# Performance work log

Measured on AMD Instinct MI355X. Metric: run time of the kernel, lower is better.

Reference implementation:

```python
import jax, jax.numpy as jnp
import numpy as np

B, F, H, W = 1, 6, 20, 26
S = F * H * W            # 3120 tokens
DIM, NH, HD = 1536, 12, 128
C = HD // 2              # 64 rotary channels
T_C = C - 2 * (C // 3)   # 22 temporal channels
H_C = C // 3             # 21
W_C = C // 3             # 21
LOCAL_FRAMES = 4         # local_attn_size (in frames)
SINK_FRAMES = 1          # sink_size (in frames)
EPS = 1e-6
MAX_POS = 1024


def _angle_table(n_ch):
    inv = 1.0 / (10000.0 ** (np.arange(n_ch, dtype=np.float64) / n_ch))
    return np.outer(np.arange(MAX_POS, dtype=np.float64), inv)


def setup_inputs() -> dict:
    key = jax.random.key(0)
    ks = jax.random.split(key, 8)
    sc = 0.02
    ang = np.concatenate([_angle_table(T_C), _angle_table(H_C), _angle_table(W_C)], axis=1)  # [1024, 64]
    return {
        "x": jax.random.normal(ks[0], (B, S, DIM), jnp.float32),
        "seq_lens": jnp.array([S], jnp.int32),
        "grid_sizes": jnp.array([[F, H, W]], jnp.int32),
        "freqs_cos": jnp.asarray(np.cos(ang), jnp.float32),
        "freqs_sin": jnp.asarray(np.sin(ang), jnp.float32),
        "Wq": jax.random.normal(ks[1], (DIM, DIM), jnp.float32) * sc,
        "bq": jnp.zeros((DIM,), jnp.float32),
        "Wk": jax.random.normal(ks[2], (DIM, DIM), jnp.float32) * sc,
        "bk": jnp.zeros((DIM,), jnp.float32),
        "Wv": jax.random.normal(ks[3], (DIM, DIM), jnp.float32) * sc,
        "bv": jnp.zeros((DIM,), jnp.float32),
        "Wo": jax.random.normal(ks[4], (DIM, DIM), jnp.float32) * sc,
        "bo": jnp.zeros((DIM,), jnp.float32),
        "gq": jnp.ones((DIM,), jnp.float32),
        "gk": jnp.ones((DIM,), jnp.float32),
    }


def _rms_norm(x, g):
    # WanRMSNorm: x * rsqrt(mean(x^2) + eps) * weight
    return x * jax.lax.rsqrt(jnp.mean(x * x, axis=-1, keepdims=True) + EPS) * g


def _rope_apply(x, freqs_cos, freqs_sin):
    # x: [B, S, NH, HD]; per-token 3D (f,h,w) rotary on consecutive pairs.
    pos = jnp.arange(S)
    f = pos // (H * W)
    hh = (pos // W) % H
    ww = pos % W
    cos_t, cos_h, cos_w = freqs_cos[:, :T_C], freqs_cos[:, T_C:T_C + H_C], freqs_cos[:, T_C + H_C:]
    sin_t, sin_h, sin_w = freqs_sin[:, :T_C], freqs_sin[:, T_C:T_C + H_C], freqs_sin[:, T_C + H_C:]
    cos = jnp.concatenate([cos_t[f], cos_h[hh], cos_w[ww]], axis=-1)[None, :, None, :]  # [1,S,1,C]
    sin = jnp.concatenate([sin_t[f], sin_h[hh], sin_w[ww]], axis=-1)[None, :, None, :]
    xp = x.reshape(B, S, NH, C, 2)
    xr, xi = xp[..., 0], xp[..., 1]
    out = jnp.stack([xr * cos - xi * sin, xr * sin + xi * cos], axis=-1)
    return out.reshape(B, S, NH, HD)


def _block_mask():
    # frame-causal + local window (in frames) + sink frames: [S, S] bool
    fid = jnp.arange(S) // (H * W)
    fi, fj = fid[:, None], fid[None, :]
    return (fj <= fi) & ((fi - fj < LOCAL_FRAMES) | (fj < SINK_FRAMES))


def reference(x, seq_lens, grid_sizes, freqs_cos, freqs_sin,
              Wq, bq, Wk, bk, Wv, bv, Wo, bo, gq, gk):
    q = _rms_norm(x @ Wq + bq, gq).reshape(B, S, NH, HD)
    k = _rms_norm(x @ Wk + bk, gk).reshape(B, S, NH, HD)
    v = (x @ Wv + bv).reshape(B, S, NH, HD)
    rq = _rope_apply(q, freqs_cos, freqs_sin)
    rk = _rope_apply(k, freqs_cos, freqs_sin)
    scale = 1.0 / jnp.sqrt(jnp.asarray(HD, x.dtype))
    scores = jnp.einsum('bind,bjnd->bnij', rq, rk) * scale  # [B,NH,S,S]
    scores = jnp.where(_block_mask()[None, None], scores, jnp.finfo(scores.dtype).min)
    attn = jax.nn.softmax(scores, axis=-1)
    out = jnp.einsum('bnij,bjnd->bind', attn, v).reshape(B, S, DIM)
    return out @ Wo + bo
```

## Files before the change

### kernel.cpp

```cpp
#include <hip/hip_runtime.h>
#include <hip/hip_bf16.h>
#include <stdint.h>

typedef short v8s __attribute__((ext_vector_type(8)));
typedef float v4f __attribute__((ext_vector_type(4)));
typedef unsigned short u16;

#define S_LEN 3120
#define DIMN 1536
#define NHEAD 12
#define HDIM 128
#define FRM 520
#define NT128 25
#define TASKS_PH 86
#define TOTAL_TASKS 1032
#define SCALE_QK 0.088388347648318447f
#define MAXOFF 12.0f

__device__ __forceinline__ v4f mfma16(v8s a, v8s b, v4f c) {
  return __builtin_amdgcn_mfma_f32_16x16x32_bf16(a, b, c, 0, 0, 0);
}
__device__ __forceinline__ float b2f(u16 u) {
  union { float f; unsigned int i; } x; x.i = ((unsigned int)u) << 16; return x.f;
}
__device__ __forceinline__ u16 f2b(float f) {
  union { float f; unsigned int i; } x; x.f = f;
  unsigned int r = x.i + 0x7FFFu + ((x.i >> 16) & 1u);
  return (u16)(r >> 16);
}
__device__ __forceinline__ void async16(const void* g, void* l) {
  __builtin_amdgcn_global_load_lds(
      (__attribute__((address_space(1))) const void*)g,
      (__attribute__((address_space(3))) void*)l, 16, 0, 0);
}

__global__ void detect_dtype(const u16* __restrict__ w, int* __restrict__ flag) {
  __shared__ int sh;
  int t = threadIdx.x;
  if (t == 0) sh = 0;
  __syncthreads();
  u16 m0 = (u16)(w[2 * t] & 0x7FFF);
  u16 m1 = (u16)(w[2 * t + 1] & 0x7FFF);
  if (m0 >= 0x4480 || m1 >= 0x4480) atomicOr(&sh, 1);
  __syncthreads();
  if (t == 0) *flag = sh;
}

struct ConvArgs { const void* src[9]; u16* dst[9]; int n[9]; };
__global__ __launch_bounds__(256) void convert_all(ConvArgs a, const int* __restrict__ flag) {
  int id = blockIdx.y;
  int n = a.n[id];
  int isf = *flag;
  const float* sf = (const float*)a.src[id];
  const u16* sb = (const u16*)a.src[id];
  u16* d = a.dst[id];
  for (int i = blockIdx.x * 256 + threadIdx.x; i < n; i += gridDim.x * 256)
    d[i] = isf ? f2b(sf[i]) : sb[i];
}

struct TPArgs { const void* in[4]; u16* out[4]; };
__global__ __launch_bounds__(256) void transpose_conv4(TPArgs a, const int* __restrict__ flag) {
  __shared__ u16 tile[32][33];
  int z = blockIdx.z;
  const float* inf = (const float*)a.in[z];
  const u16* inb = (const u16*)a.in[z];
  u16* out = a.out[z];
  int isf = *flag;
  int t = threadIdx.x, tx = t & 31, ty = t >> 5;
  int gr0 = blockIdx.y * 32, gc0 = blockIdx.x * 32;
#pragma unroll
  for (int i = 0; i < 4; ++i) {
    int r = ty + i * 8;
    size_t idx = (size_t)(gr0 + r) * DIMN + gc0 + tx;
    tile[r][tx] = isf ? f2b(inf[idx]) : inb[idx];
  }
  __syncthreads();
#pragma unroll
  for (int i = 0; i < 4; ++i) {
    int r = ty + i * 8;
    out[(size_t)(gc0 + r) * DIMN + gr0 + tx] = tile[tx][r];
  }
}

__global__ __launch_bounds__(256) void transpose16(const u16* __restrict__ in,
                                                   u16* __restrict__ out,
                                                   int rows, int cols) {
  __shared__ u16 tile[32][33];
  int t = threadIdx.x;
  int tx = t & 31, ty = t >> 5;
  int gr0 = blockIdx.y * 32, gc0 = blockIdx.x * 32;
#pragma unroll
  for (int i = 0; i < 4; ++i) {
    int r = ty + i * 8;
    int gr = gr0 + r, gc = gc0 + tx;
    if (gr < rows && gc < cols) tile[r][tx] = in[(size_t)gr * cols + gc];
  }
  __syncthreads();
#pragma unroll
  for (int i = 0; i < 4; ++i) {
    int r = ty + i * 8;
    int orow = gc0 + r, ocol = gr0 + tx;
    if (orow < cols && ocol < rows) out[(size_t)orow * rows + ocol] = tile[tx][r];
  }
}

template <int MT>
__global__ __launch_bounds__(256) void gemm3(
    const u16* __restrict__ A,
    const u16* BT0, const u16* BT1, const u16* BT2,
    const u16* b0, const u16* b1, const u16* b2,
    void* C0, void* C1, void* C2, int M, const int* __restrict__ flag, int dyn) {
  const u16* BT; const u16* bias; void* C;
  if (blockIdx.z == 0)      { BT = BT0; bias = b0; C = C0; }
  else if (blockIdx.z == 1) { BT = BT1; bias = b1; C = C1; }
  else                      { BT = BT2; bias = b2; C = C2; }
  int f32out = dyn ? *flag : 0;
  __shared__ __align__(16) short As[MT * 64];
  __shared__ __align__(16) short Bs[128 * 64];
  int t = threadIdx.x, w = t >> 6, l = t & 63;
  int ln = l & 15, lg = l >> 4;
  int m0 = blockIdx.y * MT, n0 = blockIdx.x * 128;
  int lr = l >> 3;
  int gl = (l & 7) ^ lr;
  constexpr int ACH = MT / 32;
  const u16* gAp[ACH]; short* lAp[ACH];
#pragma unroll
  for (int i = 0; i < ACH; ++i) {
    int c = w * ACH + i;
    int arow = min(m0 + c * 8 + lr, M - 1);
    gAp[i] = A + (size_t)arow * DIMN + gl * 8;
    lAp[i] = As + c * 512;
  }
  const u16* gBp[4]; short* lBp[4];
#pragma unroll
  for (int i = 0; i < 4; ++i) {
    int c = w * 4 + i;
    int brow = n0 + c * 8 + lr;
    gBp[i] = BT + (size_t)brow * DIMN + gl * 8;
    lBp[i] = Bs + c * 512;
  }
  constexpr int NJ = (MT == 128) ? 4 : 2;
  int wm = (MT == 128) ? (w & 1) : 0;
  int wn = (MT == 128) ? (w >> 1) : w;
  int aoff[2][4], boff[2][NJ];
#pragma unroll
  for (int ks = 0; ks < 2; ++ks) {
#pragma unroll
    for (int i = 0; i < 4; ++i) {
      int ar = wm * 64 + i * 16 + ln;
      aoff[ks][i] = ar * 64 + (((ks * 4 + lg) ^ (ar & 7)) * 8);
    }
#pragma unroll
    for (int j = 0; j < NJ; ++j) {
      int br = wn * (NJ * 16) + j * 16 + ln;
      boff[ks][j] = br * 64 + (((ks * 4 + lg) ^ (br & 7)) * 8);
    }
  }
  v4f acc[4][NJ] = {};
  for (int k0 = 0; k0 < DIMN; k0 += 64) {
    __syncthreads();
#pragma unroll
    for (int i = 0; i < ACH; ++i) async16(gAp[i] + k0, lAp[i]);
#pragma unroll
    for (int i = 0; i < 4; ++i) async16(gBp[i] + k0, lBp[i]);
    __syncthreads();
#pragma unroll
    for (int ks = 0; ks < 2; ++ks) {
      v8s af[4], bfr[NJ];
#pragma unroll
      for (int i = 0; i < 4; ++i) af[i] = *(const v8s*)(As + aoff[ks][i]);
#pragma unroll
      for (int j = 0; j < NJ; ++j) bfr[j] = *(const v8s*)(Bs + boff[ks][j]);
#pragma unroll
      for (int i = 0; i < 4; ++i)
#pragma unroll
        for (int j = 0; j < NJ; ++j) acc[i][j] = mfma16(af[i], bfr[j], acc[i][j]);
    }
  }
#pragma unroll
  for (int i = 0; i < 4; ++i) {
    int rb = m0 + wm * 64 + i * 16 + lg * 4;
#pragma unroll
    for (int j = 0; j < NJ; ++j) {
      int col = n0 + wn * (NJ * 16) + j * 16 + ln;
      float bv = b2f(bias[col]);
#pragma unroll
      for (int r = 0; r < 4; ++r) {
        int grow = rb + r;
        if (grow < M) {
          size_t idx = (size_t)grow * DIMN + col;
          float val = acc[i][j][r] + bv;
          if (f32out) ((float*)C)[idx] = val;
          else        ((u16*)C)[idx] = f2b(val);
        }
      }
    }
  }
}

__global__ __launch_bounds__(256) void norm_rope(u16* __restrict__ Q, u16* __restrict__ K,
                                                 const u16* __restrict__ gq,
                                                 const u16* __restrict__ gk,
                                                 const u16* __restrict__ fcos,
                                                 const u16* __restrict__ fsin) {
  int s = blockIdx.x;
  u16* base = (blockIdx.y == 0 ? Q : K) + (size_t)s * DIMN;
  const u16* g = (blockIdx.y == 0) ? gq : gk;
  int t = threadIdx.x;
  int e = t * 6;
  float x[6];
#pragma unroll
  for (int i = 0; i < 6; ++i) x[i] = b2f(base[e + i]);
  float ss = 0.f;
#pragma unroll
  for (int i = 0; i < 6; ++i) ss += x[i] * x[i];
#pragma unroll
  for (int off = 32; off > 0; off >>= 1) ss += __shfl_xor(ss, off);
  __shared__ float red[4];
  if ((t & 63) == 0) red[t >> 6] = ss;
  __syncthreads();
  float tot = red[0] + red[1] + red[2] + red[3];
  float rs = rsqrtf(tot * (1.0f / DIMN) + 1e-6f);
  int f = s / FRM;
  int hh = (s / 26) % 20;
  int ww = s % 26;
#pragma unroll
  for (int u = 0; u < 3; ++u) {
    int e0 = e + 2 * u;
    int c = (e0 & 127) >> 1;
    int p = (c < 22) ? f : ((c < 43) ? hh : ww);
    float co = b2f(fcos[p * 64 + c]);
    float si = b2f(fsin[p * 64 + c]);
    float xr = x[2 * u] * rs * b2f(g[e0]);
    float xi = x[2 * u + 1] * rs * b2f(g[e0 + 1]);
    base[e0]     = f2b(xr * co - xi * si);
    base[e0 + 1] = f2b(xr * si + xi * co);
  }
}

__global__ __launch_bounds__(256) void attn_block(const u16* __restrict__ Q,
                                                  const u16* __restrict__ K,
                                                  const u16* __restrict__ VT,
                                                  u16* __restrict__ Po,
                                                  float* __restrict__ Pl) {
  __shared__ __align__(16) short Ks[64 * 128];
  __shared__ __align__(16) short Vs[128 * 64];
  __shared__ __align__(16) short Pt[4][32 * 72];
  int t = threadIdx.x, w = t >> 6, l = t & 63;
  int ln = l & 15, lg = l >> 4;
  int task = blockIdx.x;
  int head = task / TASKS_PH, tid = task % TASKS_PH;
  int tile = 0, frame = 0;
  {
    int acc = 0;
    for (tile = 0; tile < NT128; ++tile) {
      int q0t = tile * 128;
      int f_lo = q0t / FRM;
      int f_hi = min(q0t + 127, S_LEN - 1) / FRM;
      int fstart = max(0, f_lo - 3);
      int sink = fstart > 0;
      int nf = f_hi - fstart + 1 + sink;
      if (tid < acc + nf) {
        int c = tid - acc;
        frame = sink ? (c == 0 ? 0 : fstart + c - 1) : (fstart + c);
        break;
      }
      acc += nf;
    }
  }
  int q0 = tile * 128 + w * 32;
  v8s qf[2][4];
  bool rowok[2][4];
#pragma unroll
  for (int g = 0; g < 2; ++g) {
    int row = min(q0 + g * 16 + ln, S_LEN - 1);
    const u16* qp = Q + (size_t)row * DIMN + head * HDIM + lg * 8;
#pragma unroll
    for (int c = 0; c < 4; ++c) qf[g][c] = *(const v8s*)(qp + c * 32);
#pragma unroll
    for (int r = 0; r < 4; ++r) {
      int qr = q0 + g * 16 + lg * 4 + r;
      int fi = (qr < S_LEN) ? qr / FRM : -1;
      rowok[g][r] = (frame <= fi) && ((fi - frame) < 4 || frame == 0);
    }
  }
  float lsum[2][4] = {};
  v4f o[2][8] = {};
  int kbeg = frame * FRM, kend = kbeg + FRM;
  for (int kb = kbeg; kb < kend; kb += 64) {
    __syncthreads();
#pragma unroll
    for (int i = 0; i < 4; ++i) {
      int c = w * 4 + i;
      int n = c * 64 + l;
      int r = n >> 4;
      int gl = (n & 15) ^ (r & 15);
      int krow = min(kb + r, S_LEN - 1);
      async16((const char*)K + (size_t)krow * (DIMN * 2) + head * 256 + gl * 16,
              (char*)Ks + c * 1024);
    }
#pragma unroll
    for (int i = 0; i < 4; ++i) {
      int c = w * 4 + i;
      int n = c * 64 + l;
      int d = n >> 3;
      int gl = (n & 7) ^ (d & 7);
      async16((const char*)VT + (size_t)(head * HDIM + d) * (S_LEN * 2) + (size_t)kb * 2 + gl * 16,
              (char*)Vs + c * 1024);
    }
    __syncthreads();
    v4f s[2][4] = {};
#pragma unroll
    for (int kg = 0; kg < 4; ++kg) {
      int kr = kg * 16 + ln;
#pragma unroll
      for (int c = 0; c < 4; ++c) {
        v8s kf = *(const v8s*)(Ks + kr * 128 + (((c * 4 + lg) ^ ln) * 8));
        s[0][kg] = mfma16(qf[0][c], kf, s[0][kg]);
        s[1][kg] = mfma16(qf[1][c], kf, s[1][kg]);
      }
    }
#pragma unroll
    for (int g = 0; g < 2; ++g)
#pragma unroll
      for (int kg = 0; kg < 4; ++kg) {
        bool jv = (kb + kg * 16 + ln) < kend;
#pragma unroll
        for (int r = 0; r < 4; ++r) {
          float p = (rowok[g][r] && jv) ? __expf(s[g][kg][r] * SCALE_QK - MAXOFF) : 0.f;
          lsum[g][r] += p;
          Pt[w][(g * 16 + lg * 4 + r) * 72 + kg * 16 + ln] = f2b(p);
        }
      }
#pragma unroll
    for (int kc = 0; kc < 2; ++kc) {
      v8s pf0 = *(const v8s*)(&Pt[w][ln * 72 + kc * 32 + lg * 8]);
      v8s pf1 = *(const v8s*)(&Pt[w][(16 + ln) * 72 + kc * 32 + lg * 8]);
#pragma unroll
      for (int d = 0; d < 8; ++d) {
        int rr = d * 16 + ln;
        v8s vf = *(const v8s*)(Vs + rr * 64 + (((kc * 4 + lg) ^ (ln & 7)) * 8));
        o[0][d] = mfma16(pf0, vf, o[0][d]);
        o[1][d] = mfma16(pf1, vf, o[1][d]);
      }
    }
  }
#pragma unroll
  for (int g = 0; g < 2; ++g)
#pragma unroll
    for (int r = 0; r < 4; ++r) {
      float v = lsum[g][r];
      v += __shfl_xor(v, 1);
      v += __shfl_xor(v, 2);
      v += __shfl_xor(v, 4);
      v += __shfl_xor(v, 8);
      lsum[g][r] = v;
    }
  size_t pbase = (size_t)task * (128 * 128);
#pragma unroll
  for (int g = 0; g < 2; ++g)
#pragma unroll
    for (int d = 0; d < 8; ++d)
#pragma unroll
      for (int r = 0; r < 4; ++r) {
        int lrow = w * 32 + g * 16 + lg * 4 + r;
        Po[pbase + lrow * 128 + d * 16 + ln] = f2b(o[g][d][r]);
      }
  if (ln == 0) {
#pragma unroll
    for (int g = 0; g < 2; ++g)
#pragma unroll
      for (int r = 0; r < 4; ++r)
        Pl[task * 128 + w * 32 + g * 16 + lg * 4 + r] = lsum[g][r];
  }
}

__global__ __launch_bounds__(256) void attn_combine(const u16* __restrict__ Po,
                                                    const float* __restrict__ Pl,
                                                    u16* __restrict__ Oa) {
  int tile = blockIdx.x, h = blockIdx.y;
  int accv = 0, nf = 0;
  for (int q = 0; q < NT128; ++q) {
    int q0t = q * 128;
    int f_lo = q0t / FRM;
    int f_hi = min(q0t + 127, S_LEN - 1) / FRM;
    int fstart = max(0, f_lo - 3);
    int sink = fstart > 0;
    nf = f_hi - fstart + 1 + sink;
    if (q == tile) break;
    accv += nf;
  }
  int base = h * TASKS_PH + accv;
  int t = threadIdx.x;
  int row = t >> 1, seg = (t & 1) * 64;
  int grow = tile * 128 + row;
  if (grow >= S_LEN) return;
  float lsum = 0.f;
  float ao[64];
#pragma unroll
  for (int j = 0; j < 64; ++j) ao[j] = 0.f;
  for (int c = 0; c < nf; ++c) {
    int task = base + c;
    lsum += Pl[task * 128 + row];
    const u16* p = Po + (size_t)task * 16384 + row * 128 + seg;
#pragma unroll
    for (int v = 0; v < 8; ++v) {
      v8s x = *(const v8s*)(p + v * 8);
#pragma unroll
      for (int j = 0; j < 8; ++j) ao[v * 8 + j] += b2f((u16)x[j]);
    }
  }
  float inv = 1.0f / lsum;
  u16* dst = Oa + (size_t)grow * DIMN + h * HDIM + seg;
#pragma unroll
  for (int v = 0; v < 8; ++v) {
    v8s res;
#pragma unroll
    for (int j = 0; j < 8; ++j) res[j] = (short)f2b(ao[v * 8 + j] * inv);
    *(v8s*)(dst + v * 8) = res;
  }
}

extern "C" void kernel_launch(void* const* d_in, const int* in_sizes, int n_in,
                              void* d_out, int out_size, void* d_ws, size_t ws_size,
                              hipStream_t stream) {
  (void)n_in; (void)out_size; (void)ws_size;
  int* flag = (int*)d_ws;
  u16* ws = (u16*)d_ws;
  size_t off = 16;
  const size_t SD = (size_t)S_LEN * DIMN;
  const size_t WW = (size_t)DIMN * DIMN;
  const size_t NPO = (size_t)TOTAL_TASKS * 128 * 128;
  auto alloc = [&](size_t n) { u16* p = ws + off; off += (n + 7) & ~(size_t)7; return p; };
  u16* Xc  = alloc(SD);
  u16* Fc  = alloc(65536);
  u16* Fs  = alloc(65536);
  u16* bqc = alloc(1536); u16* bkc = alloc(1536); u16* bvc = alloc(1536); u16* boc = alloc(1536);
  u16* gqc = alloc(1536); u16* gkc = alloc(1536);
  u16* Qr = alloc(SD); u16* Kr = alloc(SD); u16* Vr = alloc(SD); u16* Oa = alloc(SD);
  u16* WoT = alloc(WW);
  u16* WqT = alloc(WW); u16* WkT = alloc(WW); u16* WvT = alloc(WW);
  alloc(NPO - 3 * WW);
  float* Pl = (float*)alloc((size_t)TOTAL_TASKS * 128 * 2);
  u16* Po = WqT;
  u16* VT = Xc;

  detect_dtype<<<1, 256, 0, stream>>>((const u16*)d_in[5], flag);

  ConvArgs ca;
  const int srcIdx[9] = {0, 3, 4, 6, 8, 10, 12, 13, 14};
  u16* dsts[9] = {Xc, Fc, Fs, bqc, bkc, bvc, boc, gqc, gkc};
  for (int i = 0; i < 9; ++i) {
    ca.src[i] = d_in[srcIdx[i]];
    ca.dst[i] = dsts[i];
    ca.n[i] = in_sizes[srcIdx[i]];
  }
  convert_all<<<dim3(512, 9), 256, 0, stream>>>(ca, flag);

  TPArgs tp;
  tp.in[0] = d_in[5];  tp.out[0] = WqT;
  tp.in[1] = d_in[7];  tp.out[1] = WkT;
  tp.in[2] = d_in[9];  tp.out[2] = WvT;
  tp.in[3] = d_in[11]; tp.out[3] = WoT;
  dim3 b256(256);
  transpose_conv4<<<dim3(48, 48, 4), b256, 0, stream>>>(tp, flag);
  gemm3<64><<<dim3(12, 49, 3), b256, 0, stream>>>(Xc, WqT, WkT, WvT, bqc, bkc, bvc,
                                                  Qr, Kr, Vr, S_LEN, flag, 0);
  norm_rope<<<dim3(S_LEN, 2), b256, 0, stream>>>(Qr, Kr, gqc, gkc, Fc, Fs);
  transpose16<<<dim3(48, 98), b256, 0, stream>>>(Vr, VT, S_LEN, DIMN);
  attn_block<<<dim3(TOTAL_TASKS), b256, 0, stream>>>(Qr, Kr, VT, Po, Pl);
  attn_combine<<<dim3(NT128, NHEAD), b256, 0, stream>>>(Po, Pl, Oa);
  gemm3<64><<<dim3(12, 49, 1), b256, 0, stream>>>(Oa, WoT, WoT, WoT, boc, boc, boc,
                                                  d_out, d_out, d_out, S_LEN, flag, 1);
}
```

Measured before the change: 401.7 us.

## Shrink attention query tiles to 64 rows and key steps to 32; merge prep kernels

Attention tasks now cover 64-query tiles with 2 waves (128 threads) instead of 128-query tiles with 4 waves, and iterate keys in 32-row steps with smaller LDS buffers. This roughly doubles the task count to improve load balance and occupancy, and shrinks the partial-output buffers. The sum is accumulated from the truncated bf16 probabilities so it matches the values fed to the MFMA. The conversion and transpose prep kernels are merged into one launch. Per-task Q loads and K/V reuse drop, so more global traffic per output is the risk.

New measurement: 375.2 us. -6.6%, faster.

```diff
diff --git a/kernel.cpp b/kernel.cpp
--- a/kernel.cpp
+++ b/kernel.cpp
@@ -11,9 +11,10 @@
 #define NHEAD 12
 #define HDIM 128
 #define FRM 520
-#define NT128 25
-#define TASKS_PH 86
-#define TOTAL_TASKS 1032
+#define NT64 49
+#define T64_PH 166
+#define TOT64 1992
+#define NSTEP32 17
 #define SCALE_QK 0.088388347648318447f
 #define MAXOFF 12.0f
 
@@ -46,39 +47,43 @@
   if (t == 0) *flag = sh;
 }
 
-struct ConvArgs { const void* src[9]; u16* dst[9]; int n[9]; };
-__global__ __launch_bounds__(256) void convert_all(ConvArgs a, const int* __restrict__ flag) {
-  int id = blockIdx.y;
-  int n = a.n[id];
+struct PrepArgs {
+  const void* tin[4]; u16* tout[4];
+  const void* csrc[9]; u16* cdst[9]; int cn[9];
+};
+__global__ __launch_bounds__(256) void prep(PrepArgs a, const int* __restrict__ flag) {
   int isf = *flag;
-  const float* sf = (const float*)a.src[id];
-  const u16* sb = (const u16*)a.src[id];
-  u16* d = a.dst[id];
-  for (int i = blockIdx.x * 256 + threadIdx.x; i < n; i += gridDim.x * 256)
-    d[i] = isf ? f2b(sf[i]) : sb[i];
-}
-
-struct TPArgs { const void* in[4]; u16* out[4]; };
-__global__ __launch_bounds__(256) void transpose_conv4(TPArgs a, const int* __restrict__ flag) {
-  __shared__ u16 tile[32][33];
   int z = blockIdx.z;
-  const float* inf = (const float*)a.in[z];
-  const u16* inb = (const u16*)a.in[z];
-  u16* out = a.out[z];
-  int isf = *flag;
-  int t = threadIdx.x, tx = t & 31, ty = t >> 5;
-  int gr0 = blockIdx.y * 32, gc0 = blockIdx.x * 32;
-#pragma unroll
-  for (int i = 0; i < 4; ++i) {
-    int r = ty + i * 8;
-    size_t idx = (size_t)(gr0 + r) * DIMN + gc0 + tx;
-    tile[r][tx] = isf ? f2b(inf[idx]) : inb[idx];
-  }
-  __syncthreads();
-#pragma unroll
-  for (int i = 0; i < 4; ++i) {
-    int r = ty + i * 8;
-    out[(size_t)(gc0 + r) * DIMN + gr0 + tx] = tile[tx][r];
+  int t = threadIdx.x;
+  if (z < 4) {
+    __shared__ u16 tile[32][33];
+    const float* inf = (const float*)a.tin[z];
+    const u16* inb = (const u16*)a.tin[z];
+    u16* out = a.tout[z];
+    int tx = t & 31, ty = t >> 5;
+    int gr0 = blockIdx.y * 32, gc0 = blockIdx.x * 32;
+#pragma unroll
+    for (int i = 0; i < 4; ++i) {
+      int r = ty + i * 8;
+      size_t idx = (size_t)(gr0 + r) * DIMN + gc0 + tx;
+      tile[r][tx] = isf ? f2b(inf[idx]) : inb[idx];
+    }
+    __syncthreads();
+#pragma unroll
+    for (int i = 0; i < 4; ++i) {
+      int r = ty + i * 8;
+      out[(size_t)(gc0 + r) * DIMN + gr0 + tx] = tile[tx][r];
+    }
+  } else {
+    int id = z - 4;
+    int n = a.cn[id];
+    const float* sf = (const float*)a.csrc[id];
+    const u16* sb = (const u16*)a.csrc[id];
+    u16* d = a.cdst[id];
+    int bidx = blockIdx.y * gridDim.x + blockIdx.x;
+    int stride = gridDim.x * gridDim.y * 256;
+    for (int i = bidx * 256 + t; i < n; i += stride)
+      d[i] = isf ? f2b(sf[i]) : sb[i];
   }
 }
 
@@ -238,25 +243,25 @@
   }
 }
 
-__global__ __launch_bounds__(256) void attn_block(const u16* __restrict__ Q,
+__global__ __launch_bounds__(128) void attn_block(const u16* __restrict__ Q,
                                                   const u16* __restrict__ K,
                                                   const u16* __restrict__ VT,
                                                   u16* __restrict__ Po,
                                                   float* __restrict__ Pl) {
-  __shared__ __align__(16) short Ks[64 * 128];
-  __shared__ __align__(16) short Vs[128 * 64];
-  __shared__ __align__(16) short Pt[4][32 * 72];
+  __shared__ __align__(16) short Ks[32 * 128];
+  __shared__ __align__(16) short Vs[128 * 32];
+  __shared__ __align__(16) short Pt[2][32 * 40];
   int t = threadIdx.x, w = t >> 6, l = t & 63;
   int ln = l & 15, lg = l >> 4;
   int task = blockIdx.x;
-  int head = task / TASKS_PH, tid = task % TASKS_PH;
+  int head = task / T64_PH, tid = task % T64_PH;
   int tile = 0, frame = 0;
   {
     int acc = 0;
-    for (tile = 0; tile < NT128; ++tile) {
-      int q0t = tile * 128;
+    for (tile = 0; tile < NT64; ++tile) {
+      int q0t = tile * 64;
       int f_lo = q0t / FRM;
-      int f_hi = min(q0t + 127, S_LEN - 1) / FRM;
+      int f_hi = min(q0t + 63, S_LEN - 1) / FRM;
       int fstart = max(0, f_lo - 3);
       int sink = fstart > 0;
       int nf = f_hi - fstart + 1 + sink;
@@ -268,7 +273,7 @@
       acc += nf;
     }
   }
-  int q0 = tile * 128 + w * 32;
+  int q0 = tile * 64 + w * 32;
   v8s qf[2][4];
   bool rowok[2][4];
 #pragma unroll
@@ -287,35 +292,34 @@
   float lsum[2][4] = {};
   v4f o[2][8] = {};
   int kbeg = frame * FRM, kend = kbeg + FRM;
-  for (int kb = kbeg; kb < kend; kb += 64) {
+  int kr_i[4], kgl_i[4], vd_i[4], vgl_i[4];
+#pragma unroll
+  for (int i = 0; i < 4; ++i) {
+    int n = (w * 4 + i) * 64 + l;
+    kr_i[i] = n >> 4;
+    kgl_i[i] = (n & 15) ^ (kr_i[i] & 15);
+    vd_i[i] = n >> 2;
+    vgl_i[i] = (n & 3) ^ (vd_i[i] & 3);
+  }
+  const u16* Kb = K + head * HDIM;
+  for (int it = 0; it < NSTEP32; ++it) {
+    int kb = kbeg + it * 32;
     __syncthreads();
 #pragma unroll
     for (int i = 0; i < 4; ++i) {
-      int c = w * 4 + i;
-      int n = c * 64 + l;
-      int r = n >> 4;
-      int gl = (n & 15) ^ (r & 15);
-      int krow = min(kb + r, S_LEN - 1);
-      async16((const char*)K + (size_t)krow * (DIMN * 2) + head * 256 + gl * 16,
-              (char*)Ks + c * 1024);
-    }
-#pragma unroll
-    for (int i = 0; i < 4; ++i) {
-      int c = w * 4 + i;
-      int n = c * 64 + l;
-      int d = n >> 3;
-      int gl = (n & 7) ^ (d & 7);
-      async16((const char*)VT + (size_t)(head * HDIM + d) * (S_LEN * 2) + (size_t)kb * 2 + gl * 16,
-              (char*)Vs + c * 1024);
+      int krow = min(kb + kr_i[i], S_LEN - 1);
+      async16(Kb + (size_t)krow * DIMN + kgl_i[i] * 8,
+              (char*)Ks + (size_t)(w * 4 + i) * 1024);
+      async16(VT + (size_t)(head * HDIM + vd_i[i]) * S_LEN + kb + vgl_i[i] * 8,
+              (char*)Vs + (size_t)(w * 4 + i) * 1024);
     }
     __syncthreads();
-    v4f s[2][4] = {};
-#pragma unroll
-    for (int kg = 0; kg < 4; ++kg) {
-      int kr = kg * 16 + ln;
+    v4f s[2][2] = {};
+#pragma unroll
+    for (int kg = 0; kg < 2; ++kg) {
 #pragma unroll
       for (int c = 0; c < 4; ++c) {
-        v8s kf = *(const v8s*)(Ks + kr * 128 + (((c * 4 + lg) ^ ln) * 8));
+        v8s kf = *(const v8s*)(&Ks[(kg * 16 + ln) * 128 + (((c * 4 + lg) ^ ln) * 8)]);
         s[0][kg] = mfma16(qf[0][c], kf, s[0][kg]);
         s[1][kg] = mfma16(qf[1][c], kf, s[1][kg]);
       }
@@ -323,26 +327,24 @@
 #pragma unroll
     for (int g = 0; g < 2; ++g)
 #pragma unroll
-      for (int kg = 0; kg < 4; ++kg) {
+      for (int kg = 0; kg < 2; ++kg) {
         bool jv = (kb + kg * 16 + ln) < kend;
 #pragma unroll
         for (int r = 0; r < 4; ++r) {
           float p = (rowok[g][r] && jv) ? __expf(s[g][kg][r] * SCALE_QK - MAXOFF) : 0.f;
-          lsum[g][r] += p;
-          Pt[w][(g * 16 + lg * 4 + r) * 72 + kg * 16 + ln] = f2b(p);
+          unsigned int bi = __float_as_uint(p) & 0xffff0000u;
+          lsum[g][r] += __uint_as_float(bi);
+          Pt[w][(g * 16 + lg * 4 + r) * 40 + kg * 16 + ln] = (u16)(bi >> 16);
         }
       }
-#pragma unroll
-    for (int kc = 0; kc < 2; ++kc) {
-      v8s pf0 = *(const v8s*)(&Pt[w][ln * 72 + kc * 32 + lg * 8]);
-      v8s pf1 = *(const v8s*)(&Pt[w][(16 + ln) * 72 + kc * 32 + lg * 8]);
-#pragma unroll
-      for (int d = 0; d < 8; ++d) {
-        int rr = d * 16 + ln;
-        v8s vf = *(const v8s*)(Vs + rr * 64 + (((kc * 4 + lg) ^ (ln & 7)) * 8));
-        o[0][d] = mfma16(pf0, vf, o[0][d]);
-        o[1][d] = mfma16(pf1, vf, o[1][d]);
-      }
+    v8s pf0 = *(const v8s*)(&Pt[w][ln * 40 + lg * 8]);
+    v8s pf1 = *(const v8s*)(&Pt[w][(16 + ln) * 40 + lg * 8]);
+#pragma unroll
+    for (int d = 0; d < 8; ++d) {
+      int rr = d * 16 + ln;
+      v8s vf = *(const v8s*)(&Vs[rr * 32 + ((lg ^ (rr & 3)) * 8)]);
+      o[0][d] = mfma16(pf0, vf, o[0][d]);
+      o[1][d] = mfma16(pf1, vf, o[1][d]);
     }
   }
 #pragma unroll
@@ -356,7 +358,7 @@
       v += __shfl_xor(v, 8);
       lsum[g][r] = v;
     }
-  size_t pbase = (size_t)task * (128 * 128);
+  size_t pbase = (size_t)task * (64 * 128);
 #pragma unroll
   for (int g = 0; g < 2; ++g)
 #pragma unroll
@@ -371,7 +373,7 @@
     for (int g = 0; g < 2; ++g)
 #pragma unroll
       for (int r = 0; r < 4; ++r)
-        Pl[task * 128 + w * 32 + g * 16 + lg * 4 + r] = lsum[g][r];
+        Pl[task * 64 + w * 32 + g * 16 + lg * 4 + r] = lsum[g][r];
   }
 }
 
@@ -380,31 +382,31 @@
                                                     u16* __restrict__ Oa) {
   int tile = blockIdx.x, h = blockIdx.y;
   int accv = 0, nf = 0;
-  for (int q = 0; q < NT128; ++q) {
-    int q0t = q * 128;
+  for (int q = 0; q < NT64; ++q) {
+    int q0t = q * 64;
     int f_lo = q0t / FRM;
-    int f_hi = min(q0t + 127, S_LEN - 1) / FRM;
+    int f_hi = min(q0t + 63, S_LEN - 1) / FRM;
     int fstart = max(0, f_lo - 3);
     int sink = fstart > 0;
     nf = f_hi - fstart + 1 + sink;
     if (q == tile) break;
     accv += nf;
   }
-  int base = h * TASKS_PH + accv;
+  int base = h * T64_PH + accv;
   int t = threadIdx.x;
-  int row = t >> 1, seg = (t & 1) * 64;
-  int grow = tile * 128 + row;
+  int row = t >> 2, seg = (t & 3) * 32;
+  int grow = tile * 64 + row;
   if (grow >= S_LEN) return;
   float lsum = 0.f;
-  float ao[64];
-#pragma unroll
-  for (int j = 0; j < 64; ++j) ao[j] = 0.f;
+  float ao[32];
+#pragma unroll
+  for (int j = 0; j < 32; ++j) ao[j] = 0.f;
   for (int c = 0; c < nf; ++c) {
     int task = base + c;
-    lsum += Pl[task * 128 + row];
-    const u16* p = Po + (size_t)task * 16384 + row * 128 + seg;
-#pragma unroll
-    for (int v = 0; v < 8; ++v) {
+    lsum += Pl[task * 64 + row];
+    const u16* p = Po + (size_t)task * 8192 + row * 128 + seg;
+#pragma unroll
+    for (int v = 0; v < 4; ++v) {
       v8s x = *(const v8s*)(p + v * 8);
 #pragma unroll
       for (int j = 0; j < 8; ++j) ao[v * 8 + j] += b2f((u16)x[j]);
@@ -413,7 +415,7 @@
   float inv = 1.0f / lsum;
   u16* dst = Oa + (size_t)grow * DIMN + h * HDIM + seg;
 #pragma unroll
-  for (int v = 0; v < 8; ++v) {
+  for (int v = 0; v < 4; ++v) {
     v8s res;
 #pragma unroll
     for (int j = 0; j < 8; ++j) res[j] = (short)f2b(ao[v * 8 + j] * inv);
@@ -430,7 +432,7 @@
   size_t off = 16;
   const size_t SD = (size_t)S_LEN * DIMN;
   const size_t WW = (size_t)DIMN * DIMN;
-  const size_t NPO = (size_t)TOTAL_TASKS * 128 * 128;
+  const size_t NPO = (size_t)1032 * 128 * 128;
   auto alloc = [&](size_t n) { u16* p = ws + off; off += (n + 7) & ~(size_t)7; return p; };
   u16* Xc  = alloc(SD);
   u16* Fc  = alloc(65536);
@@ -441,35 +443,32 @@
   u16* WoT = alloc(WW);
   u16* WqT = alloc(WW); u16* WkT = alloc(WW); u16* WvT = alloc(WW);
   alloc(NPO - 3 * WW);
-  float* Pl = (float*)alloc((size_t)TOTAL_TASKS * 128 * 2);
+  float* Pl = (float*)alloc((size_t)TOT64 * 64 * 2);
   u16* Po = WqT;
   u16* VT = Xc;
 
   detect_dtype<<<1, 256, 0, stream>>>((const u16*)d_in[5], flag);
 
-  ConvArgs ca;
+  PrepArgs pa;
+  pa.tin[0] = d_in[5];  pa.tout[0] = WqT;
+  pa.tin[1] = d_in[7];  pa.tout[1] = WkT;
+  pa.tin[2] = d_in[9];  pa.tout[2] = WvT;
+  pa.tin[3] = d_in[11]; pa.tout[3] = WoT;
   const int srcIdx[9] = {0, 3, 4, 6, 8, 10, 12, 13, 14};
   u16* dsts[9] = {Xc, Fc, Fs, bqc, bkc, bvc, boc, gqc, gkc};
   for (int i = 0; i < 9; ++i) {
-    ca.src[i] = d_in[srcIdx[i]];
-    ca.dst[i] = dsts[i];
-    ca.n[i] = in_sizes[srcIdx[i]];
-  }
-  convert_all<<<dim3(512, 9), 256, 0, stream>>>(ca, flag);
-
-  TPArgs tp;
-  tp.in[0] = d_in[5];  tp.out[0] = WqT;
-  tp.in[1] = d_in[7];  tp.out[1] = WkT;
-  tp.in[2] = d_in[9];  tp.out[2] = WvT;
-  tp.in[3] = d_in[11]; tp.out[3] = WoT;
+    pa.csrc[i] = d_in[srcIdx[i]];
+    pa.cdst[i] = dsts[i];
+    pa.cn[i] = in_sizes[srcIdx[i]];
+  }
   dim3 b256(256);
-  transpose_conv4<<<dim3(48, 48, 4), b256, 0, stream>>>(tp, flag);
+  prep<<<dim3(48, 48, 13), b256, 0, stream>>>(pa, flag);
   gemm3<64><<<dim3(12, 49, 3), b256, 0, stream>>>(Xc, WqT, WkT, WvT, bqc, bkc, bvc,
                                                   Qr, Kr, Vr, S_LEN, flag, 0);
   norm_rope<<<dim3(S_LEN, 2), b256, 0, stream>>>(Qr, Kr, gqc, gkc, Fc, Fs);
   transpose16<<<dim3(48, 98), b256, 0, stream>>>(Vr, VT, S_LEN, DIMN);
-  attn_block<<<dim3(TOTAL_TASKS), b256, 0, stream>>>(Qr, Kr, VT, Po, Pl);
-  attn_combine<<<dim3(NT128, NHEAD), b256, 0, stream>>>(Po, Pl, Oa);
+  attn_block<<<dim3(TOT64), dim3(128), 0, stream>>>(Qr, Kr, VT, Po, Pl);
+  attn_combine<<<dim3(NT64, NHEAD), b256, 0, stream>>>(Po, Pl, Oa);
   gemm3<64><<<dim3(12, 49, 1), b256, 0, stream>>>(Oa, WoT, WoT, WoT, boc, boc, boc,
                                                   d_out, d_out, d_out, S_LEN, flag, 1);
 }
```
